# Kernel optimization log

Hardware: AMD Instinct MI355X
Metric: run time of the kernel (lower is better)

The kernel has to match this reference:

```python
import jax, jax.numpy as jnp
import numpy as np

RANK = 32
BASE_RES = 4


def interp_matrix(n_out, r):
    # align_corners=True bilinear sampling of an r-point axis at cell-centered
    # coords (i+0.5)/n_out mapped to [-1,1]; t = (i+0.5)/n_out * (r-1).
    t = (jnp.arange(n_out, dtype=jnp.float32) + 0.5) / n_out * (r - 1)
    i0 = jnp.clip(jnp.floor(t), 0, r - 2).astype(jnp.int32)
    frac = t - i0.astype(jnp.float32)
    w = (jax.nn.one_hot(i0, r, dtype=jnp.float32) * (1.0 - frac)[:, None]
         + jax.nn.one_hot(i0 + 1, r, dtype=jnp.float32) * frac[:, None])
    return w  # (n_out, r)


def setup_inputs() -> dict:
    key = jax.random.key(0)
    ks = jax.random.split(key, 6)
    B, Cin, Cout, H, W = 8, 128, 128, 128, 128
    fan_in = Cin * BASE_RES * BASE_RES
    stdv = 1.0 / np.sqrt(Cin)
    v = jax.random.normal(ks[0], (B, Cin, H, W), dtype=jnp.float32)
    k1 = jax.random.normal(ks[1], (RANK, Cin, BASE_RES, BASE_RES), dtype=jnp.float32) / np.sqrt(fan_in)
    k2 = jax.random.normal(ks[2], (RANK, Cout, BASE_RES, BASE_RES), dtype=jnp.float32) / np.sqrt(fan_in)
    conv_w = jax.random.uniform(ks[3], (Cout, Cin), dtype=jnp.float32, minval=-stdv, maxval=stdv)
    conv_b = jax.random.uniform(ks[4], (Cout,), dtype=jnp.float32, minval=-stdv, maxval=stdv)
    bias = jax.random.uniform(ks[5], (Cout, 1, 1), dtype=jnp.float32, minval=-stdv, maxval=stdv)
    return {"v": v, "k1": k1, "k2": k2, "conv_w": conv_w, "conv_b": conv_b, "bias": bias}


def reference(v, k1, k2, conv_w, conv_b, bias):
    B, Cin, H, W = v.shape
    r = k1.shape[-1]
    wy = interp_matrix(H, r)  # (H, r)
    wx = interp_matrix(W, r)  # (W, r)
    # grid_sample(kernel, cell-centered grid, align_corners=True, bilinear)
    k1i = jnp.einsum('hp,wq,ripq->rihw', wy, wx, k1)  # (R, Cin, H, W)
    k2i = jnp.einsum('hp,wq,ropq->rohw', wy, wx, k2)  # (R, Cout, H, W)
    vr = jnp.einsum('rihw,bihw->br', k1i, v) / (H * W)  # (B, R)
    out = jnp.einsum('rohw,br->bohw', k2i, vr)          # (B, Cout, H, W)
    out = out + jnp.einsum('oi,bihw->bohw', conv_w, v) + conv_b[None, :, None, None]
    out = out + bias[None]
    return out
```

## Files before the change

kernel.cpp:

```cpp
#include <hip/hip_runtime.h>


__global__ __launch_bounds__(256) void kA_reduceS(const float* __restrict__ v,
                                                  float* __restrict__ S)
{
    int bid = blockIdx.x;
    const float* img = v + ((size_t)bid << 14);
    int tid  = threadIdx.x;
    int wave = tid >> 6, lane = tid & 63;

    int w0 = lane * 2;
    float wxA[4], wxB[4];
    {
        float t0 = (w0 + 0.5f) * (3.0f / 128.0f);
        int j0 = (int)t0; j0 = j0 > 2 ? 2 : j0;
        float f0 = t0 - (float)j0;
        float t1 = (w0 + 1.5f) * (3.0f / 128.0f);
        int j1 = (int)t1; j1 = j1 > 2 ? 2 : j1;
        float f1 = t1 - (float)j1;
#pragma unroll
        for (int q = 0; q < 4; ++q) {
            wxA[q] = (q == j0) ? (1.0f - f0) : ((q == j0 + 1) ? f0 : 0.0f);
            wxB[q] = (q == j1) ? (1.0f - f1) : ((q == j1 + 1) ? f1 : 0.0f);
        }
    }

    float acc[4][4] = {};
#pragma unroll 4
    for (int h = wave; h < 128; h += 4) {
        float2 px = *(const float2*)(img + h * 128 + w0);
        float part[4];
#pragma unroll
        for (int q = 0; q < 4; ++q) part[q] = px.x * wxA[q] + px.y * wxB[q];
        float t = (h + 0.5f) * (3.0f / 128.0f);
        int i0 = (int)t; i0 = i0 > 2 ? 2 : i0;
        float fr = t - (float)i0;
#pragma unroll
        for (int p = 0; p < 4; ++p) {
            float wyp = (p == i0) ? (1.0f - fr) : ((p == i0 + 1) ? fr : 0.0f);
#pragma unroll
            for (int q = 0; q < 4; ++q) acc[p][q] += wyp * part[q];
        }
    }

#pragma unroll
    for (int p = 0; p < 4; ++p)
#pragma unroll
        for (int q = 0; q < 4; ++q) {
            float s = acc[p][q];
#pragma unroll
            for (int m = 32; m >= 1; m >>= 1) s += __shfl_xor(s, m, 64);
            acc[p][q] = s;
        }

    __shared__ float red[4][16];
    if (lane == 0) {
#pragma unroll
        for (int p = 0; p < 4; ++p)
#pragma unroll
            for (int q = 0; q < 4; ++q) red[wave][p * 4 + q] = acc[p][q];
    }
    __syncthreads();
    if (tid < 16) {
        float s = red[0][tid] + red[1][tid] + red[2][tid] + red[3][tid];
        S[(bid << 4) + tid] = s;
    }
}

__global__ __launch_bounds__(256) void kB_small(const float* __restrict__ S,
                                                const float* __restrict__ k1,
                                                const float* __restrict__ k2,
                                                const float* __restrict__ conv_w,
                                                const float* __restrict__ conv_b,
                                                const float* __restrict__ bias,
                                                float* __restrict__ T,
                                                float* __restrict__ Wt)
{
    int b = blockIdx.x;
    int tid = threadIdx.x;
    __shared__ float Ss[2048];
    __shared__ float vrs[32];

    const float* Sb = S + b * 2048;
#pragma unroll
    for (int it = 0; it < 2; ++it) {
        int f = (it * 256 + tid) * 4;
        *(float4*)&Ss[f] = *(const float4*)&Sb[f];
    }
    __syncthreads();

    {
        int r = tid >> 3, j = tid & 7;
        const float* k1r = k1 + r * 2048 + j * 256;
        const float* Sj  = Ss + j * 256;
        float partial = 0.0f;
#pragma unroll 4
        for (int e = 0; e < 256; e += 4) {
            float4 a  = *(const float4*)&k1r[e];
            float4 s4 = *(const float4*)&Sj[e];
            partial += a.x * s4.x + a.y * s4.y + a.z * s4.z + a.w * s4.w;
        }
        partial += __shfl_xor(partial, 1, 64);
        partial += __shfl_xor(partial, 2, 64);
        partial += __shfl_xor(partial, 4, 64);
        if (j == 0) vrs[r] = partial * (1.0f / 16384.0f);
    }
    __syncthreads();

    {
        int f0 = tid * 8;
        int o  = tid >> 1;
        float cb = conv_b[o] + bias[o];
        float acc[8] = {};
        for (int rr = 0; rr < 32; ++rr) {
            float vv = vrs[rr];
            const float* k2r = k2 + rr * 2048 + f0;
            float4 a0 = *(const float4*)&k2r[0];
            float4 a1 = *(const float4*)&k2r[4];
            acc[0] += vv * a0.x; acc[1] += vv * a0.y;
            acc[2] += vv * a0.z; acc[3] += vv * a0.w;
            acc[4] += vv * a1.x; acc[5] += vv * a1.y;
            acc[6] += vv * a1.z; acc[7] += vv * a1.w;
        }
        float* Tb = T + b * 2048 + f0;
        float4 r0, r1;
        r0.x = acc[0] + cb; r0.y = acc[1] + cb; r0.z = acc[2] + cb; r0.w = acc[3] + cb;
        r1.x = acc[4] + cb; r1.y = acc[5] + cb; r1.z = acc[6] + cb; r1.w = acc[7] + cb;
        *(float4*)&Tb[0] = r0;
        *(float4*)&Tb[4] = r1;
    }

    {
        int o8   = (tid & 15) * 8;
        int irow = (b << 4) + (tid >> 4);
        float r[8];
#pragma unroll
        for (int j = 0; j < 8; ++j) r[j] = conv_w[(o8 + j) * 128 + irow];
        *(float4*)&Wt[irow * 128 + o8]     = *(float4*)&r[0];
        *(float4*)&Wt[irow * 128 + o8 + 4] = *(float4*)&r[4];
    }
}

__global__ __launch_bounds__(256) void kC_main(const float* __restrict__ v,
                                               const float* __restrict__ Wt,
                                               const float* __restrict__ T,
                                               float* __restrict__ out)
{
    int h = blockIdx.x;
    int b = blockIdx.y;
    int tid = threadIdx.x;

    __shared__ float Wl[32][128];
    __shared__ float Vl[32][128];
    __shared__ float U[128][4];

    float t = (h + 0.5f) * (3.0f / 128.0f);
    int i0 = (int)t; i0 = i0 > 2 ? 2 : i0;
    float fr = t - (float)i0;

    if (tid < 128) {
        const float* Tb = T + b * 2048 + tid * 16;
        float4 r0 = *(const float4*)&Tb[0];
        float4 r1 = *(const float4*)&Tb[4];
        float4 r2 = *(const float4*)&Tb[8];
        float4 r3 = *(const float4*)&Tb[12];
        float wy0 = (i0 == 0) ? (1.0f - fr) : 0.0f;
        float wy1 = (i0 == 1) ? (1.0f - fr) : ((i0 == 0) ? fr : 0.0f);
        float wy2 = (i0 == 2) ? (1.0f - fr) : ((i0 == 1) ? fr : 0.0f);
        float wy3 = (i0 == 2) ? fr : 0.0f;
        U[tid][0] = wy0 * r0.x + wy1 * r1.x + wy2 * r2.x + wy3 * r3.x;
        U[tid][1] = wy0 * r0.y + wy1 * r1.y + wy2 * r2.y + wy3 * r3.y;
        U[tid][2] = wy0 * r0.z + wy1 * r1.z + wy2 * r2.z + wy3 * r3.z;
        U[tid][3] = wy0 * r0.w + wy1 * r1.w + wy2 * r2.w + wy3 * r3.w;
    }

    float acc[8][8] = {};
    int to = tid >> 4, tn = tid & 15;
    const float* vb = v + (size_t)b * 2097152 + h * 128;

    for (int kc = 0; kc < 128; kc += 32) {
#pragma unroll
        for (int it = 0; it < 4; ++it) {
            int f  = it * 256 + tid;
            int kk = f >> 5;
            int c4 = (f & 31) << 2;
            *(float4*)&Wl[kk][c4] = *(const float4*)&Wt[(kc + kk) * 128 + c4];
            *(float4*)&Vl[kk][c4] = *(const float4*)&vb[(size_t)(kc + kk) * 16384 + c4];
        }
        __syncthreads();
#pragma unroll 4
        for (int kk = 0; kk < 32; ++kk) {
            float wf[8], vf[8];
            *(float4*)&wf[0] = *(const float4*)&Wl[kk][to * 8];
            *(float4*)&wf[4] = *(const float4*)&Wl[kk][to * 8 + 4];
            *(float4*)&vf[0] = *(const float4*)&Vl[kk][tn * 8];
            *(float4*)&vf[4] = *(const float4*)&Vl[kk][tn * 8 + 4];
#pragma unroll
            for (int m = 0; m < 8; ++m)
#pragma unroll
                for (int n = 0; n < 8; ++n)
                    acc[m][n] += wf[m] * vf[n];
        }
        __syncthreads();
    }

    float wx[8][4];
#pragma unroll
    for (int n = 0; n < 8; ++n) {
        int w = tn * 8 + n;
        float tw = (w + 0.5f) * (3.0f / 128.0f);
        int j0 = (int)tw; j0 = j0 > 2 ? 2 : j0;
        float fw = tw - (float)j0;
#pragma unroll
        for (int q = 0; q < 4; ++q)
            wx[n][q] = (q == j0) ? (1.0f - fw) : ((q == j0 + 1) ? fw : 0.0f);
    }

    float* ob = out + (size_t)b * 2097152 + h * 128 + tn * 8;
#pragma unroll
    for (int m = 0; m < 8; ++m) {
        int o = to * 8 + m;
        float4 Uo = *(const float4*)&U[o][0];
        float res[8];
#pragma unroll
        for (int n = 0; n < 8; ++n)
            res[n] = acc[m][n] + wx[n][0] * Uo.x + wx[n][1] * Uo.y
                               + wx[n][2] * Uo.z + wx[n][3] * Uo.w;
        *(float4*)&ob[(size_t)o * 16384]     = *(float4*)&res[0];
        *(float4*)&ob[(size_t)o * 16384 + 4] = *(float4*)&res[4];
    }
}

extern "C" void kernel_launch(void* const* d_in, const int* in_sizes, int n_in,
                              void* d_out, int out_size, void* d_ws, size_t ws_size,
                              hipStream_t stream) {
    const float* v      = (const float*)d_in[0];
    const float* k1     = (const float*)d_in[1];
    const float* k2     = (const float*)d_in[2];
    const float* conv_w = (const float*)d_in[3];
    const float* conv_b = (const float*)d_in[4];
    const float* bias   = (const float*)d_in[5];
    float* out = (float*)d_out;

    float* S  = (float*)d_ws;
    float* T  = S + 16384;
    float* Wt = T + 16384;

    kA_reduceS<<<1024, 256, 0, stream>>>(v, S);
    kB_small<<<8, 256, 0, stream>>>(S, k1, k2, conv_w, conv_b, bias, T, Wt);
    kC_main<<<dim3(128, 8), 256, 0, stream>>>(v, Wt, T, out);
}
```

Measured before the change: 191.3 us.

## Replace FP32 FMA channel-mix GEMM with split-bf16 MFMA and swizzled LDS

The 1x1 conv GEMM in the main kernel now runs on bf16 MFMA instructions. The weights are split into hi and lo bf16 halves in the small kernel, pre-packed into fragment order, and applied with two MFMAs per tile. The activation tile is converted to bf16 and stored transposed in LDS with an XOR swizzle to avoid bank conflicts. This removes the scalar FP32 FMA bottleneck, at the cost of rounding v to bf16, which loses precision on the activation side. Output stores become scalar per lane rather than float4.

```diff
diff --git a/kernel.cpp b/kernel.cpp
--- a/kernel.cpp
+++ b/kernel.cpp
@@ -1,5 +1,20 @@
 #include <hip/hip_runtime.h>
 
+
+typedef __attribute__((ext_vector_type(8))) short bf16x8;
+typedef __attribute__((ext_vector_type(4))) float f32x4;
+typedef unsigned int u32;
+typedef unsigned short u16;
+
+static __device__ __forceinline__ u16 f2bf(float x) {
+    union { float f; u32 u; } a; a.f = x;
+    u32 r = a.u + 0x7fffu + ((a.u >> 16) & 1u);
+    return (u16)(r >> 16);
+}
+static __device__ __forceinline__ float bf2f(u16 h) {
+    union { u32 u; float f; } a; a.u = ((u32)h) << 16;
+    return a.f;
+}
 
 __global__ __launch_bounds__(256) void kA_reduceS(const float* __restrict__ v,
                                                   float* __restrict__ S)
@@ -74,7 +89,8 @@
                                                 const float* __restrict__ conv_b,
                                                 const float* __restrict__ bias,
                                                 float* __restrict__ T,
-                                                float* __restrict__ Wt)
+                                                u16* __restrict__ Wh,
+                                                u16* __restrict__ Wl)
 {
     int b = blockIdx.x;
     int tid = threadIdx.x;
@@ -131,103 +147,142 @@
     }
 
     {
-        int o8   = (tid & 15) * 8;
-        int irow = (b << 4) + (tid >> 4);
-        float r[8];
-#pragma unroll
-        for (int j = 0; j < 8; ++j) r[j] = conv_w[(o8 + j) * 128 + irow];
-        *(float4*)&Wt[irow * 128 + o8]     = *(float4*)&r[0];
-        *(float4*)&Wt[irow * 128 + o8 + 4] = *(float4*)&r[4];
-    }
-}
-
-__global__ __launch_bounds__(256) void kC_main(const float* __restrict__ v,
-                                               const float* __restrict__ Wt,
-                                               const float* __restrict__ T,
-                                               float* __restrict__ out)
+        int ks = tid >> 6, l = tid & 63;
+        int o = (b << 4) + (l & 15);
+        int ibase = ks * 32 + ((l >> 4) << 3);
+        const float* src = conv_w + o * 128 + ibase;
+        float4 c0 = *(const float4*)src;
+        float4 c1 = *(const float4*)(src + 4);
+        float xs[8] = {c0.x, c0.y, c0.z, c0.w, c1.x, c1.y, c1.z, c1.w};
+        union { u16 s[8]; bf16x8 v; } ph, pl;
+#pragma unroll
+        for (int j = 0; j < 8; ++j) {
+            u16 hi = f2bf(xs[j]);
+            ph.s[j] = hi;
+            pl.s[j] = f2bf(xs[j] - bf2f(hi));
+        }
+        int didx = (((b * 4 + ks) * 64) + l) * 8;
+        *(bf16x8*)(Wh + didx) = ph.v;
+        *(bf16x8*)(Wl + didx) = pl.v;
+    }
+}
+
+__global__ __launch_bounds__(256, 4) void kC_mfma(const float* __restrict__ v,
+                                                  const u16* __restrict__ Wh,
+                                                  const u16* __restrict__ Wl,
+                                                  const float* __restrict__ T,
+                                                  float* __restrict__ out)
 {
-    int h = blockIdx.x;
-    int b = blockIdx.y;
+    __shared__ u16 vt[16384];
+    __shared__ float U[128][4];
+
+    int h = blockIdx.x, b = blockIdx.y;
     int tid = threadIdx.x;
-
-    __shared__ float Wl[32][128];
-    __shared__ float Vl[32][128];
-    __shared__ float U[128][4];
-
-    float t = (h + 0.5f) * (3.0f / 128.0f);
-    int i0 = (int)t; i0 = i0 > 2 ? 2 : i0;
-    float fr = t - (float)i0;
-
-    if (tid < 128) {
-        const float* Tb = T + b * 2048 + tid * 16;
-        float4 r0 = *(const float4*)&Tb[0];
-        float4 r1 = *(const float4*)&Tb[4];
-        float4 r2 = *(const float4*)&Tb[8];
-        float4 r3 = *(const float4*)&Tb[12];
-        float wy0 = (i0 == 0) ? (1.0f - fr) : 0.0f;
-        float wy1 = (i0 == 1) ? (1.0f - fr) : ((i0 == 0) ? fr : 0.0f);
-        float wy2 = (i0 == 2) ? (1.0f - fr) : ((i0 == 1) ? fr : 0.0f);
-        float wy3 = (i0 == 2) ? fr : 0.0f;
-        U[tid][0] = wy0 * r0.x + wy1 * r1.x + wy2 * r2.x + wy3 * r3.x;
-        U[tid][1] = wy0 * r0.y + wy1 * r1.y + wy2 * r2.y + wy3 * r3.y;
-        U[tid][2] = wy0 * r0.z + wy1 * r1.z + wy2 * r2.z + wy3 * r3.z;
-        U[tid][3] = wy0 * r0.w + wy1 * r1.w + wy2 * r2.w + wy3 * r3.w;
-    }
-
-    float acc[8][8] = {};
-    int to = tid >> 4, tn = tid & 15;
-    const float* vb = v + (size_t)b * 2097152 + h * 128;
-
-    for (int kc = 0; kc < 128; kc += 32) {
-#pragma unroll
-        for (int it = 0; it < 4; ++it) {
-            int f  = it * 256 + tid;
-            int kk = f >> 5;
-            int c4 = (f & 31) << 2;
-            *(float4*)&Wl[kk][c4] = *(const float4*)&Wt[(kc + kk) * 128 + c4];
-            *(float4*)&Vl[kk][c4] = *(const float4*)&vb[(size_t)(kc + kk) * 16384 + c4];
-        }
-        __syncthreads();
-#pragma unroll 4
-        for (int kk = 0; kk < 32; ++kk) {
-            float wf[8], vf[8];
-            *(float4*)&wf[0] = *(const float4*)&Wl[kk][to * 8];
-            *(float4*)&wf[4] = *(const float4*)&Wl[kk][to * 8 + 4];
-            *(float4*)&vf[0] = *(const float4*)&Vl[kk][tn * 8];
-            *(float4*)&vf[4] = *(const float4*)&Vl[kk][tn * 8 + 4];
-#pragma unroll
-            for (int m = 0; m < 8; ++m)
-#pragma unroll
-                for (int n = 0; n < 8; ++n)
-                    acc[m][n] += wf[m] * vf[n];
-        }
-        __syncthreads();
-    }
-
-    float wx[8][4];
-#pragma unroll
-    for (int n = 0; n < 8; ++n) {
-        int w = tn * 8 + n;
-        float tw = (w + 0.5f) * (3.0f / 128.0f);
+    int lane = tid & 63, wid = tid >> 6;
+
+    const float* vb = v + ((size_t)b << 21) + h * 128;
+
+    {
+        int w = tid & 127, ib = tid >> 7;
+        unsigned sw = (unsigned)(w & 15);
+        unsigned rowbase = (unsigned)w * 256 + (unsigned)ib * 8;
+#pragma unroll
+        for (int it = 0; it < 16; ++it) {
+            int i0 = it * 8 + ib * 4;
+            float x0 = vb[(size_t)(i0 + 0) * 16384 + w];
+            float x1 = vb[(size_t)(i0 + 1) * 16384 + w];
+            float x2 = vb[(size_t)(i0 + 2) * 16384 + w];
+            float x3 = vb[(size_t)(i0 + 3) * 16384 + w];
+            u32 p0 = (u32)f2bf(x0) | ((u32)f2bf(x1) << 16);
+            u32 p1 = (u32)f2bf(x2) | ((u32)f2bf(x3) << 16);
+            unsigned byteoff = rowbase + ((((unsigned)it) ^ sw) << 4);
+            *(uint2*)((char*)vt + byteoff) = make_uint2(p0, p1);
+        }
+    }
+
+    {
+        float t = (h + 0.5f) * (3.0f / 128.0f);
+        int i0 = (int)t; i0 = i0 > 2 ? 2 : i0;
+        float fr = t - (float)i0;
+        if (tid < 128) {
+            const float* Tb = T + b * 2048 + tid * 16;
+            float4 r0 = *(const float4*)&Tb[0];
+            float4 r1 = *(const float4*)&Tb[4];
+            float4 r2 = *(const float4*)&Tb[8];
+            float4 r3 = *(const float4*)&Tb[12];
+            float wy0 = (i0 == 0) ? (1.0f - fr) : 0.0f;
+            float wy1 = (i0 == 1) ? (1.0f - fr) : ((i0 == 0) ? fr : 0.0f);
+            float wy2 = (i0 == 2) ? (1.0f - fr) : ((i0 == 1) ? fr : 0.0f);
+            float wy3 = (i0 == 2) ? fr : 0.0f;
+            U[tid][0] = wy0 * r0.x + wy1 * r1.x + wy2 * r2.x + wy3 * r3.x;
+            U[tid][1] = wy0 * r0.y + wy1 * r1.y + wy2 * r2.y + wy3 * r3.y;
+            U[tid][2] = wy0 * r0.z + wy1 * r1.z + wy2 * r2.z + wy3 * r3.z;
+            U[tid][3] = wy0 * r0.w + wy1 * r1.w + wy2 * r2.w + wy3 * r3.w;
+        }
+    }
+    __syncthreads();
+
+    int mh = wid >> 1, nh = wid & 1;
+    int g = lane >> 4, ln = lane & 15;
+
+    f32x4 acc[4][4];
+#pragma unroll
+    for (int mt = 0; mt < 4; ++mt)
+#pragma unroll
+        for (int nt = 0; nt < 4; ++nt)
+            acc[mt][nt] = (f32x4){0.f, 0.f, 0.f, 0.f};
+
+#pragma unroll
+    for (int ks = 0; ks < 4; ++ks) {
+        bf16x8 Ah[4], Al[4];
+#pragma unroll
+        for (int mt = 0; mt < 4; ++mt) {
+            int idx = ((((mh * 4 + mt) * 4 + ks) * 64) + lane) * 8;
+            Ah[mt] = *(const bf16x8*)(Wh + idx);
+            Al[mt] = *(const bf16x8*)(Wl + idx);
+        }
+#pragma unroll
+        for (int nt = 0; nt < 4; ++nt) {
+            unsigned wrow = (unsigned)(nh * 64 + nt * 16 + ln);
+            unsigned byteoff = wrow * 256 + ((((unsigned)(ks * 4 + g)) ^ (unsigned)ln) << 4);
+            bf16x8 Bf = *(const bf16x8*)((const char*)vt + byteoff);
+#pragma unroll
+            for (int mt = 0; mt < 4; ++mt) {
+                acc[mt][nt] = __builtin_amdgcn_mfma_f32_16x16x32_bf16(Ah[mt], Bf, acc[mt][nt], 0, 0, 0);
+                acc[mt][nt] = __builtin_amdgcn_mfma_f32_16x16x32_bf16(Al[mt], Bf, acc[mt][nt], 0, 0, 0);
+            }
+        }
+    }
+
+    float wqa[4][4];
+#pragma unroll
+    for (int nt = 0; nt < 4; ++nt) {
+        int wn = nh * 64 + nt * 16 + ln;
+        float tw = (wn + 0.5f) * (3.0f / 128.0f);
         int j0 = (int)tw; j0 = j0 > 2 ? 2 : j0;
         float fw = tw - (float)j0;
-#pragma unroll
-        for (int q = 0; q < 4; ++q)
-            wx[n][q] = (q == j0) ? (1.0f - fw) : ((q == j0 + 1) ? fw : 0.0f);
-    }
-
-    float* ob = out + (size_t)b * 2097152 + h * 128 + tn * 8;
-#pragma unroll
-    for (int m = 0; m < 8; ++m) {
-        int o = to * 8 + m;
-        float4 Uo = *(const float4*)&U[o][0];
-        float res[8];
-#pragma unroll
-        for (int n = 0; n < 8; ++n)
-            res[n] = acc[m][n] + wx[n][0] * Uo.x + wx[n][1] * Uo.y
-                               + wx[n][2] * Uo.z + wx[n][3] * Uo.w;
-        *(float4*)&ob[(size_t)o * 16384]     = *(float4*)&res[0];
-        *(float4*)&ob[(size_t)o * 16384 + 4] = *(float4*)&res[4];
+        wqa[nt][0] = (j0 == 0) ? (1.0f - fw) : 0.0f;
+        wqa[nt][1] = (j0 == 1) ? (1.0f - fw) : ((j0 == 0) ? fw : 0.0f);
+        wqa[nt][2] = (j0 == 2) ? (1.0f - fw) : ((j0 == 1) ? fw : 0.0f);
+        wqa[nt][3] = (j0 == 2) ? fw : 0.0f;
+    }
+
+    float* ob = out + ((size_t)b << 21) + h * 128;
+#pragma unroll
+    for (int mt = 0; mt < 4; ++mt) {
+#pragma unroll
+        for (int r = 0; r < 4; ++r) {
+            int o = mh * 64 + mt * 16 + g * 4 + r;
+            float4 Uo = *(const float4*)&U[o][0];
+            float* orow = ob + (size_t)o * 16384;
+#pragma unroll
+            for (int nt = 0; nt < 4; ++nt) {
+                int wn = nh * 64 + nt * 16 + ln;
+                float res = acc[mt][nt][r] + wqa[nt][0] * Uo.x + wqa[nt][1] * Uo.y
+                                           + wqa[nt][2] * Uo.z + wqa[nt][3] * Uo.w;
+                orow[wn] = res;
+            }
+        }
     }
 }
 
@@ -244,9 +299,10 @@
 
     float* S  = (float*)d_ws;
     float* T  = S + 16384;
-    float* Wt = T + 16384;
+    u16*   Wh = (u16*)((char*)d_ws + 131072);
+    u16*   Wl = (u16*)((char*)d_ws + 163840);
 
     kA_reduceS<<<1024, 256, 0, stream>>>(v, S);
-    kB_small<<<8, 256, 0, stream>>>(S, k1, k2, conv_w, conv_b, bias, T, Wt);
-    kC_main<<<dim3(128, 8), 256, 0, stream>>>(v, Wt, T, out);
-}
+    kB_small<<<8, 256, 0, stream>>>(S, k1, k2, conv_w, conv_b, bias, T, Wh, Wl);
+    kC_mfma<<<dim3(128, 8), 256, 0, stream>>>(v, Wh, Wl, T, out);
+}
```

New measurement: 155.8 us. -18.6%, faster.
